# Performance work log

Measured on AMD Instinct MI355X. Metric: run time of the kernel, lower is better.

Reference implementation:

```python
import jax, jax.numpy as jnp
import numpy as np


def setup_inputs() -> dict:
    key = jax.random.key(0)
    B, S, H, O, L, NH = 16, 1024, 1024, 256, 4, 8
    ks = jax.random.split(key, 10)
    s = 0.02
    return {
        "x": jax.random.normal(ks[0], (B, S, H), dtype=jnp.float32),
        "Wf": jax.random.normal(ks[1], (L, H, H), dtype=jnp.float32) * s,
        "bf": jnp.zeros((L, H), dtype=jnp.float32),
        "Wi": jax.random.normal(ks[2], (L, H, H), dtype=jnp.float32) * s,
        "bi": jnp.zeros((L, H), dtype=jnp.float32),
        "Wh": jax.random.normal(ks[3], (L, H, H), dtype=jnp.float32) * s,
        "bh": jnp.zeros((L, H), dtype=jnp.float32),
        "in_proj_w": jax.random.normal(ks[4], (3 * H, H), dtype=jnp.float32) * s,
        "in_proj_b": jnp.zeros((3 * H,), dtype=jnp.float32),
        "out_w": jax.random.normal(ks[5], (H, H), dtype=jnp.float32) * s,
        "out_b": jnp.zeros((H,), dtype=jnp.float32),
        "fc_w": jax.random.normal(ks[6], (O, H), dtype=jnp.float32) * s,
        "fc_b": jnp.zeros((O,), dtype=jnp.float32),
    }


def _min_lstm_layer(x, Wf, bf, Wi, bi, Wh, bh):
    # x: [B, S, D] -> [B, S, H]. minLSTM: h_t = f'_t * h_{t-1} + i'_t * h~_t
    f = jax.nn.sigmoid(jnp.einsum("bsd,hd->bsh", x, Wf) + bf)
    i = jax.nn.sigmoid(jnp.einsum("bsd,hd->bsh", x, Wi) + bi)
    h_tilde = jnp.einsum("bsd,hd->bsh", x, Wh) + bh
    denom = f + i
    fp = f / denom                      # decay coefficient per step
    add = (i / denom) * h_tilde         # input contribution per step
    # sequential scan over time (linear gated recurrence)
    def step(h, inp):
        fp_t, add_t = inp               # each [B, H]
        h = fp_t * h + add_t
        return h, h
    B, S, H = fp.shape
    h0 = jnp.zeros((B, H), dtype=x.dtype)
    _, hs = jax.lax.scan(step, h0, (fp.transpose(1, 0, 2), add.transpose(1, 0, 2)))
    return hs.transpose(1, 0, 2)        # [B, S, H]


def _mhsa(x, in_proj_w, in_proj_b, out_w, out_b, num_heads=8):
    B, S, H = x.shape
    dh = H // num_heads
    qkv = jnp.einsum("bsh,oh->bso", x, in_proj_w) + in_proj_b  # [B,S,3H]
    q, k, v = jnp.split(qkv, 3, axis=-1)
    def heads(t):
        return t.reshape(B, S, num_heads, dh).transpose(0, 2, 1, 3)  # [B,nh,S,dh]
    q, k, v = heads(q), heads(k), heads(v)
    scores = jnp.einsum("bnqd,bnkd->bnqk", q, k) / jnp.sqrt(jnp.float32(dh)).astype(x.dtype)
    attn = jax.nn.softmax(scores, axis=-1)
    o = jnp.einsum("bnqk,bnkd->bnqd", attn, v)
    o = o.transpose(0, 2, 1, 3).reshape(B, S, H)
    return jnp.einsum("bsh,oh->bso", o, out_w) + out_b


def reference(x, Wf, bf, Wi, bi, Wh, bh, in_proj_w, in_proj_b, out_w, out_b, fc_w, fc_b):
    out = x
    L = Wf.shape[0]
    for l in range(L):
        out = _min_lstm_layer(out, Wf[l], bf[l], Wi[l], bi[l], Wh[l], bh[l])
    attn_out = _mhsa(out, in_proj_w, in_proj_b, out_w, out_b, num_heads=8)
    out = attn_out + out                 # dropout is identity at eval
    last = out[:, -1, :]                 # [B, H]
    return jnp.einsum("bh,oh->bo", last, fc_w) + fc_b
```

## Files before the change

### kernel.cpp

```cpp
#include <hip/hip_runtime.h>
#include <hip/hip_bf16.h>
#include <math.h>

#define Bq   16
#define Sq   1024
#define Hq   1024
#define Oq   256
#define Lq   4
#define NHq  8
#define DHq  128
#define Mq   (Bq*Sq)
#define HHq  (Hq*Hq)
#define NCc  32
#define CTc  32

typedef __bf16 bf16x8 __attribute__((ext_vector_type(8)));
typedef float  f32x4  __attribute__((ext_vector_type(4)));

__device__ __forceinline__ float bf2f(unsigned int u) {
    union { unsigned int i; float f; } x; x.i = u << 16; return x.f;
}
__device__ __forceinline__ unsigned short f2bf(float f) {
    union { float f; unsigned int i; } x; x.f = f;
    unsigned int r = x.i + 0x7fffu + ((x.i >> 16) & 1u);
    return (unsigned short)(r >> 16);
}
__device__ __forceinline__ float sigm(float x) { return 1.f / (1.f + __expf(-x)); }

__device__ __forceinline__ void gl2lds16(const unsigned short* g, unsigned short* l) {
    __builtin_amdgcn_global_load_lds((const __attribute__((address_space(1))) void*)g,
                                     (__attribute__((address_space(3))) void*)l, 16, 0, 0);
}

__global__ void cvt_kernel(const float* __restrict__ src, unsigned short* __restrict__ dst, int n) {
    int i = blockIdx.x * 256 + threadIdx.x;
    if (i < n) dst[i] = f2bf(src[i]);
}

__global__ void cvtW_kernel(const float* __restrict__ Wf, const float* __restrict__ Wi,
                            const float* __restrict__ Wh, unsigned short* __restrict__ Wcat) {
    int i = blockIdx.x * 256 + threadIdx.x;
    int l = (i >> 20) / 3;
    int r = i - l * 3 * HHq;
    int g = r >> 20; int j = r & (HHq - 1);
    const float* s = (g == 0) ? Wf : (g == 1) ? Wi : Wh;
    Wcat[i] = f2bf(s[(size_t)l * HHq + j]);
}

__global__ void bias3_kernel(const float* __restrict__ bf_, const float* __restrict__ bi_,
                             const float* __restrict__ bh_, float* __restrict__ out) {
    int i = blockIdx.x * 256 + threadIdx.x;
    int l = i / (3*Hq); int r = i % (3*Hq); int g = r >> 10; int j = r & (Hq-1);
    const float* s = (g == 0) ? bf_ : (g == 1) ? bi_ : bh_;
    out[i] = s[l*Hq + j];
}

__global__ __launch_bounds__(512, 1)
void gemm_gate_kernel(const unsigned short* __restrict__ A, const unsigned short* __restrict__ Wl,
                      const float* __restrict__ bias3, unsigned short* __restrict__ FPo,
                      unsigned short* __restrict__ ADDo)
{
    const int K = Hq;
    __shared__ unsigned short lds[4 * 20480];
    const int tid  = threadIdx.x;

    const int lid = blockIdx.x;
    const int xcd = lid & 7;
    const int s   = lid >> 3;
    const int bm  = xcd * 8 + (s >> 3);
    const int cb  = s & 7;

    const int wid  = tid >> 6, lane = tid & 63;
    const int wm   = (wid >> 2) * 128;
    const int wn   = (wid & 3) * 32;
    const int l15  = lane & 15, quad = lane >> 4;

    const unsigned short* Ag = A + (size_t)(bm*256) * K;

    const int lr   = lane >> 2;
    const int gc   = (lane & 3) ^ ((lane >> 3) & 3);
    int offA[2], ldsA[2];
    #pragma unroll
    for (int q = 0; q < 2; ++q) {
        int ra = wid*32 + q*16 + lr;
        offA[q] = ra * K + gc*8;
        ldsA[q] = (wid*32 + q*16) * 32;
    }
    int offW[3], ldsW[3];
    #pragma unroll
    for (int q = 0; q < 3; ++q) {
        int rw = wid*48 + q*16 + lr;
        int g  = rw >> 7;
        int nr = rw & 127;
        offW[q] = g * HHq + (cb*128 + nr) * K + gc*8;
        ldsW[q] = 8192 + (wid*48 + q*16) * 32;
    }

    const int crd = quad ^ ((l15 >> 1) & 3);

    f32x4 acc[3][8][2] = {};

    auto STAGE = [&](int kt, int slot) {
        const int kof = kt << 5;
        unsigned short* Sb = &lds[slot * 20480];
        #pragma unroll
        for (int q = 0; q < 2; ++q) gl2lds16(Ag + offA[q] + kof, Sb + ldsA[q]);
        #pragma unroll
        for (int q = 0; q < 3; ++q) gl2lds16(Wl + offW[q] + kof, Sb + ldsW[q]);
    };

    auto COMPUTE = [&](int slot) {
        const unsigned short* Sa = &lds[slot * 20480];
        const unsigned short* Sw = Sa + 8192;
        bf16x8 af[8];
        #pragma unroll
        for (int t = 0; t < 8; ++t)
            af[t] = *(const bf16x8*)&Sa[(wm + t*16 + l15)*32 + crd*8];
        __builtin_amdgcn_s_setprio(1);
        #pragma unroll
        for (int g = 0; g < 3; ++g) {
            bf16x8 wf[2];
            #pragma unroll
            for (int t = 0; t < 2; ++t)
                wf[t] = *(const bf16x8*)&Sw[(g*128 + wn + t*16 + l15)*32 + crd*8];
            #pragma unroll
            for (int tm = 0; tm < 8; ++tm)
                #pragma unroll
                for (int tn = 0; tn < 2; ++tn)
                    acc[g][tm][tn] = __builtin_amdgcn_mfma_f32_16x16x32_bf16(af[tm], wf[tn], acc[g][tm][tn], 0, 0, 0);
        }
        __builtin_amdgcn_s_setprio(0);
    };

    const int niter = K >> 5;

    STAGE(0, 0);
    STAGE(1, 1);

    for (int t = 0; t < niter - 2; ++t) {
        STAGE(t + 2, (t + 2) & 3);
        asm volatile("s_waitcnt vmcnt(10) lgkmcnt(0)" ::: "memory");
        __builtin_amdgcn_s_barrier();
        asm volatile("" ::: "memory");
        COMPUTE(t & 3);
    }
    asm volatile("s_waitcnt vmcnt(5) lgkmcnt(0)" ::: "memory");
    __builtin_amdgcn_s_barrier();
    asm volatile("" ::: "memory");
    COMPUTE((niter - 2) & 3);
    asm volatile("s_waitcnt vmcnt(0) lgkmcnt(0)" ::: "memory");
    __builtin_amdgcn_s_barrier();
    asm volatile("" ::: "memory");
    COMPUTE((niter - 1) & 3);

    #pragma unroll
    for (int tm = 0; tm < 8; ++tm) {
        int row0 = bm*256 + wm + tm*16 + quad*4;
        #pragma unroll
        for (int tn = 0; tn < 2; ++tn) {
            int col = cb*128 + wn + tn*16 + l15;
            float bf_ = bias3[col], bi_ = bias3[Hq + col], bh_ = bias3[2*Hq + col];
            #pragma unroll
            for (int r = 0; r < 4; ++r) {
                float f  = sigm(acc[0][tm][tn][r] + bf_);
                float i  = sigm(acc[1][tm][tn][r] + bi_);
                float ht = acc[2][tm][tn][r] + bh_;
                float rd = 1.f / (f + i);
                size_t off = (size_t)(row0 + r) * Hq + col;
                FPo[off]  = f2bf(f * rd);
                ADDo[off] = f2bf(i * rd * ht);
            }
        }
    }
}

__global__ __launch_bounds__(256, 2)
void gemm_bt_kernel(const unsigned short* __restrict__ A, const unsigned short* __restrict__ W,
                    const float* __restrict__ bias, unsigned short* __restrict__ C,
                    int N, int K, int nbn)
{
    __shared__ unsigned short lds[4 * 8192];
    const int tid  = threadIdx.x;

    const int lid = blockIdx.x;
    const int xcd = lid & 7;
    const int s   = lid >> 3;
    const int bm  = xcd * 16 + s / nbn;
    const int bn  = s % nbn;

    const int wid  = tid >> 6, lane = tid & 63;
    const int wm   = (wid >> 1) * 64, wn = (wid & 1) * 64;
    const int l15  = lane & 15, quad = lane >> 4;

    const unsigned short* Ag = A + (size_t)(bm*128) * K;
    const unsigned short* Wg = W + (size_t)(bn*128) * K;

    const int r0   = wid*32 + (lane >> 2);
    const int cst  = (lane & 3) ^ ((r0 >> 1) & 3);
    const int g0   = r0 * K + cst*8;
    const int g1   = (r0 + 16) * K + cst*8;
    const int lofs0 = wid*1024;
    const int lofs1 = wid*1024 + 512;

    const int crd = quad ^ ((l15 >> 1) & 3);

    f32x4 acc[4][4] = {};

    auto STAGE = [&](int kt, int slot) {
        const int kof = kt << 5;
        unsigned short* Sb = &lds[slot * 8192];
        gl2lds16(Ag + g0 + kof, Sb + lofs0);
        gl2lds16(Ag + g1 + kof, Sb + lofs1);
        gl2lds16(Wg + g0 + kof, Sb + 4096 + lofs0);
        gl2lds16(Wg + g1 + kof, Sb + 4096 + lofs1);
    };

    auto COMPUTE = [&](int slot) {
        const unsigned short* Sa = &lds[slot * 8192];
        const unsigned short* Sw = Sa + 4096;
        bf16x8 af[4], wf[4];
        #pragma unroll
        for (int t = 0; t < 4; ++t) {
            af[t] = *(const bf16x8*)&Sa[(wm + t*16 + l15)*32 + crd*8];
            wf[t] = *(const bf16x8*)&Sw[(wn + t*16 + l15)*32 + crd*8];
        }
        __builtin_amdgcn_s_setprio(1);
        #pragma unroll
        for (int tm = 0; tm < 4; ++tm)
            #pragma unroll
            for (int tn = 0; tn < 4; ++tn)
                acc[tm][tn] = __builtin_amdgcn_mfma_f32_16x16x32_bf16(af[tm], wf[tn], acc[tm][tn], 0, 0, 0);
        __builtin_amdgcn_s_setprio(0);
    };

    const int niter = K >> 5;

    STAGE(0, 0);
    STAGE(1, 1);

    for (int it = 0; it < niter - 2; ++it) {
        STAGE(it + 2, (it + 2) & 3);
        asm volatile("s_waitcnt vmcnt(8) lgkmcnt(0)" ::: "memory");
        __builtin_amdgcn_s_barrier();
        asm volatile("" ::: "memory");
        COMPUTE(it & 3);
    }
    asm volatile("s_waitcnt vmcnt(4) lgkmcnt(0)" ::: "memory");
    __builtin_amdgcn_s_barrier();
    asm volatile("" ::: "memory");
    COMPUTE((niter - 2) & 3);
    asm volatile("s_waitcnt vmcnt(0) lgkmcnt(0)" ::: "memory");
    __builtin_amdgcn_s_barrier();
    asm volatile("" ::: "memory");
    COMPUTE((niter - 1) & 3);

    #pragma unroll
    for (int tm = 0; tm < 4; ++tm) {
        int row0 = bm*128 + wm + tm*16 + quad*4;
        #pragma unroll
        for (int tn = 0; tn < 4; ++tn) {
            int col = bn*128 + wn + tn*16 + l15;
            float bv = bias[col];
            #pragma unroll
            for (int r = 0; r < 4; ++r)
                C[(size_t)(row0 + r) * N + col] = f2bf(acc[tm][tn][r] + bv);
        }
    }
}

__global__ __launch_bounds__(256)
void scan_sum_kernel(const unsigned short* __restrict__ FP, const unsigned short* __restrict__ AD,
                     float* __restrict__ Ps, float* __restrict__ Asum) {
    int bid = blockIdx.x;
    int tid = threadIdx.x;
    int b = bid >> 6; int r = bid & 63; int chunk = r >> 1; int jb = r & 1;
    int j = jb*512 + tid*2;
    size_t base = ((size_t)(b*Sq + chunk*CTc)) * Hq + j;
    float P0 = 1.f, P1 = 1.f, A0 = 0.f, A1 = 0.f;
    for (int s = 0; s < CTc; ++s) {
        size_t ro = base + (size_t)s * Hq;
        unsigned int uf = *(const unsigned int*)(FP + ro);
        unsigned int ua = *(const unsigned int*)(AD + ro);
        float fp0 = bf2f(uf & 0xffffu), fp1 = bf2f(uf >> 16);
        float ad0 = bf2f(ua & 0xffffu), ad1 = bf2f(ua >> 16);
        P0 *= fp0; A0 = fp0 * A0 + ad0;
        P1 *= fp1; A1 = fp1 * A1 + ad1;
    }
    int oi = (b*NCc + chunk)*Hq + j;
    Ps[oi] = P0; Ps[oi+1] = P1;
    Asum[oi] = A0; Asum[oi+1] = A1;
}

__global__ void scan_base_kernel(const float* __restrict__ Ps, const float* __restrict__ Asum,
                                 float* __restrict__ Hb) {
    int t = blockIdx.x * 256 + threadIdx.x;
    int b = t >> 10, j = t & 1023;
    float h = 0.f;
    for (int c = 0; c < NCc; ++c) {
        int idx = (b*NCc + c)*Hq + j;
        Hb[idx] = h;
        h = Ps[idx] * h + Asum[idx];
    }
}

__global__ __launch_bounds__(256)
void scan_out_kernel(const unsigned short* __restrict__ FP, const unsigned short* __restrict__ AD,
                     const float* __restrict__ Hb, unsigned short* __restrict__ Ho) {
    int bid = blockIdx.x;
    int tid = threadIdx.x;
    int b = bid >> 6; int r = bid & 63; int chunk = r >> 1; int jb = r & 1;
    int j = jb*512 + tid*2;
    size_t base = ((size_t)(b*Sq + chunk*CTc)) * Hq + j;
    int oi = (b*NCc + chunk)*Hq + j;
    float h0 = Hb[oi], h1 = Hb[oi+1];
    for (int s = 0; s < CTc; ++s) {
        size_t ro = base + (size_t)s * Hq;
        unsigned int uf = *(const unsigned int*)(FP + ro);
        unsigned int ua = *(const unsigned int*)(AD + ro);
        h0 = bf2f(uf & 0xffffu) * h0 + bf2f(ua & 0xffffu);
        h1 = bf2f(uf >> 16)     * h1 + bf2f(ua >> 16);
        unsigned int packed = (unsigned int)f2bf(h0) | ((unsigned int)f2bf(h1) << 16);
        *(unsigned int*)(Ho + ro) = packed;
    }
}

__global__ void xlast_kernel(const unsigned short* __restrict__ act, float* __restrict__ xl) {
    int i = blockIdx.x * 256 + threadIdx.x;
    int b = i >> 10, j = i & 1023;
    xl[i] = bf2f((unsigned int)act[((size_t)(b*Sq + Sq-1)) * Hq + j]);
}

__global__ __launch_bounds__(256)
void gemv_kernel(const float* __restrict__ W, const float* __restrict__ xv,
                 const float* __restrict__ bias, const float* __restrict__ resid,
                 float* __restrict__ out, int N) {
    int b = blockIdx.x;
    int w = threadIdx.x >> 6, lane = threadIdx.x & 63;
    int n = blockIdx.y*4 + w;
    __shared__ float xs[Hq];
    *(float4*)&xs[threadIdx.x*4] = *(const float4*)&xv[(size_t)b*Hq + threadIdx.x*4];
    __syncthreads();
    const float4* wr = (const float4*)(W + (size_t)n * Hq);
    float a = 0.f;
    #pragma unroll
    for (int c = 0; c < 4; ++c) {
        float4 wv = wr[c*64 + lane];
        float4 x4 = *(const float4*)&xs[c*256 + lane*4];
        a += wv.x*x4.x + wv.y*x4.y + wv.z*x4.z + wv.w*x4.w;
    }
    #pragma unroll
    for (int st = 32; st > 0; st >>= 1) a += __shfl_xor(a, st, 64);
    if (lane == 0) out[(size_t)b*N + n] = a + bias[n] + (resid ? resid[(size_t)b*Hq + n] : 0.f);
}

__global__ __launch_bounds__(1024)
void attn_kernel(const unsigned short* __restrict__ KV,
                 const float* __restrict__ q, float* __restrict__ o) {
    int b = blockIdx.x >> 3, nh = blockIdx.x & 7;
    int tid = threadIdx.x;
    __shared__ float qs[DHq];
    __shared__ float p[Sq];
    __shared__ float redw[16];
    __shared__ float red2[16*DHq];
    if (tid < DHq) qs[tid] = q[b*Hq + nh*DHq + tid] * 0.08838834764831845f;
    __syncthreads();

    const int g = tid >> 4, l = tid & 15;
    const unsigned short* Kb = KV + (size_t)b*Sq*2048 + nh*DHq;
    float lmax = -1e30f;
    #pragma unroll 4
    for (int it = 0; it < 16; ++it) {
        int s = it*64 + g;
        union { uint4 v; unsigned short u[8]; } kk;
        kk.v = *(const uint4*)(Kb + (size_t)s*2048 + l*8);
        float a = 0.f;
        #pragma unroll
        for (int j = 0; j < 8; ++j) a += bf2f((unsigned int)kk.u[j]) * qs[l*8 + j];
        a += __shfl_xor(a, 1, 16);
        a += __shfl_xor(a, 2, 16);
        a += __shfl_xor(a, 4, 16);
        a += __shfl_xor(a, 8, 16);
        if (l == 0) p[s] = a;
        lmax = fmaxf(lmax, a);
    }
    #pragma unroll
    for (int st = 32; st > 0; st >>= 1) lmax = fmaxf(lmax, __shfl_xor(lmax, st, 64));
    if ((tid & 63) == 0) redw[tid >> 6] = lmax;
    __syncthreads();
    float mx = redw[0];
    #pragma unroll
    for (int i = 1; i < 16; ++i) mx = fmaxf(mx, redw[i]);

    float e = __expf(p[tid] - mx);
    float ls = e;
    #pragma unroll
    for (int st = 32; st > 0; st >>= 1) ls += __shfl_xor(ls, st, 64);
    __syncthreads();
    p[tid] = e;
    if ((tid & 63) == 0) redw[tid >> 6] = ls;
    __syncthreads();
    float ssum = 0.f;
    #pragma unroll
    for (int i = 0; i < 16; ++i) ssum += redw[i];
    float inv = 1.f / ssum;

    int d2 = (tid & 63) * 2, sb = tid >> 6;
    const unsigned short* Vb = KV + (size_t)b*Sq*2048 + 1024 + nh*DHq + d2;
    float a0 = 0.f, a1 = 0.f;
    for (int s = sb*64; s < sb*64 + 64; ++s) {
        unsigned int vv = *(const unsigned int*)(Vb + (size_t)s*2048);
        float pw = p[s];
        a0 += pw * bf2f(vv & 0xffffu);
        a1 += pw * bf2f(vv >> 16);
    }
    red2[sb*DHq + d2] = a0;
    red2[sb*DHq + d2 + 1] = a1;
    __syncthreads();
    if (tid < DHq) {
        float a = 0.f;
        #pragma unroll
        for (int i = 0; i < 16; ++i) a += red2[i*DHq + tid];
        o[b*Hq + nh*DHq + tid] = a * inv;
    }
}

extern "C" void kernel_launch(void* const* d_in, const int* in_sizes, int n_in,
                              void* d_out, int out_size, void* d_ws, size_t ws_size,
                              hipStream_t stream) {
    const float* x        = (const float*)d_in[0];
    const float* Wf       = (const float*)d_in[1];
    const float* bfv      = (const float*)d_in[2];
    const float* Wi       = (const float*)d_in[3];
    const float* biv      = (const float*)d_in[4];
    const float* Wh       = (const float*)d_in[5];
    const float* bhv      = (const float*)d_in[6];
    const float* in_proj_w= (const float*)d_in[7];
    const float* in_proj_b= (const float*)d_in[8];
    const float* out_w    = (const float*)d_in[9];
    const float* out_b    = (const float*)d_in[10];
    const float* fc_w     = (const float*)d_in[11];
    const float* fc_b     = (const float*)d_in[12];
    float* outp = (float*)d_out;

    char* p = (char*)d_ws;
    auto alloc = [&](size_t bytes) -> void* {
        void* r = (void*)p; p += (bytes + 255) & ~(size_t)255; return r;
    };
    unsigned short* Wcat = (unsigned short*)alloc((size_t)Lq*3*HHq*2);
    unsigned short* Wkv  = (unsigned short*)alloc((size_t)2048*Hq*2);
    float*          Bias3= (float*)alloc((size_t)Lq*3*Hq*4);
    unsigned short* actA = (unsigned short*)alloc((size_t)Mq*Hq*2);
    unsigned short* actB = (unsigned short*)alloc((size_t)Mq*Hq*2);
    unsigned short* FPg  = (unsigned short*)alloc((size_t)Mq*Hq*2);
    unsigned short* ADDg = (unsigned short*)alloc((size_t)Mq*Hq*2);
    float* Ps   = (float*)alloc((size_t)Bq*NCc*Hq*4);
    float* Asum = (float*)alloc((size_t)Bq*NCc*Hq*4);
    float* Hb   = (float*)alloc((size_t)Bq*NCc*Hq*4);
    unsigned short* KV = FPg;
    float* xl   = (float*)alloc((size_t)Bq*Hq*4);
    float* qbuf = (float*)alloc((size_t)Bq*Hq*4);
    float* obuf = (float*)alloc((size_t)Bq*Hq*4);
    float* rbuf = (float*)alloc((size_t)Bq*Hq*4);

    cvt_kernel<<<Mq*Hq/256, 256, 0, stream>>>(x, actA, Mq*Hq);
    cvtW_kernel<<<Lq*3*HHq/256, 256, 0, stream>>>(Wf, Wi, Wh, Wcat);
    cvt_kernel<<<2048*Hq/256, 256, 0, stream>>>(in_proj_w + (size_t)Hq*Hq, Wkv, 2048*Hq);
    bias3_kernel<<<(Lq*3*Hq)/256, 256, 0, stream>>>(bfv, biv, bhv, Bias3);

    unsigned short* cur = actA;
    unsigned short* nxt = actB;
    for (int l = 0; l < Lq; ++l) {
        gemm_gate_kernel<<<(Mq/256)*(Hq/128), 512, 0, stream>>>(
            cur, Wcat + (size_t)l*3*HHq, Bias3 + l*3*Hq, FPg, ADDg);
        scan_sum_kernel<<<Bq*NCc*2, 256, 0, stream>>>(FPg, ADDg, Ps, Asum);
        scan_base_kernel<<<Bq*Hq/256, 256, 0, stream>>>(Ps, Asum, Hb);
        scan_out_kernel<<<Bq*NCc*2, 256, 0, stream>>>(FPg, ADDg, Hb, nxt);
        unsigned short* t = cur; cur = nxt; nxt = t;
    }

    gemm_bt_kernel<<<(Mq/128)*(2048/128), 256, 0, stream>>>(
        cur, Wkv, in_proj_b + Hq, KV, 2048, Hq, 2048/128);
    xlast_kernel<<<Bq*Hq/256, 256, 0, stream>>>(cur, xl);
    gemv_kernel<<<dim3(Bq, Hq/4), 256, 0, stream>>>(in_proj_w, xl, in_proj_b, nullptr, qbuf, Hq);
    attn_kernel<<<Bq*NHq, 1024, 0, stream>>>(KV, qbuf, obuf);
    gemv_kernel<<<dim3(Bq, Hq/4), 256, 0, stream>>>(out_w, obuf, out_b, xl, rbuf, Hq);
    gemv_kernel<<<dim3(Bq, Oq/4), 256, 0, stream>>>(fc_w, rbuf, fc_b, nullptr, outp, Oq);
}
```

Baseline: 842.1 us.

## Fuse chunk scan reduction into gate GEMM epilogue and interleave FP/ADD storage

The gate GEMM epilogue now computes per-32-row chunk products and accumulated sums using in-register accumulation and wave shuffles. It writes Ps/Asum directly, which removes the separate scan_sum kernel and its full re-read of the FP and ADD tensors. FP and ADD are stored interleaved as one 32-bit word, so scan_out reads both with a single vector load. The cost is more epilogue work and register pressure in the GEMM, plus strided 4-byte stores.

```diff
diff --git a/kernel.cpp b/kernel.cpp
--- a/kernel.cpp
+++ b/kernel.cpp
@@ -57,8 +57,8 @@
 
 __global__ __launch_bounds__(512, 1)
 void gemm_gate_kernel(const unsigned short* __restrict__ A, const unsigned short* __restrict__ Wl,
-                      const float* __restrict__ bias3, unsigned short* __restrict__ FPo,
-                      unsigned short* __restrict__ ADDo)
+                      const float* __restrict__ bias3, unsigned int* __restrict__ FA,
+                      float* __restrict__ Ps, float* __restrict__ Asum)
 {
     const int K = Hq;
     __shared__ unsigned short lds[4 * 20480];
@@ -153,22 +153,67 @@
     asm volatile("" ::: "memory");
     COMPUTE((niter - 1) & 3);
 
-    #pragma unroll
-    for (int tm = 0; tm < 8; ++tm) {
-        int row0 = bm*256 + wm + tm*16 + quad*4;
-        #pragma unroll
-        for (int tn = 0; tn < 2; ++tn) {
-            int col = cb*128 + wn + tn*16 + l15;
-            float bf_ = bias3[col], bi_ = bias3[Hq + col], bh_ = bias3[2*Hq + col];
+    const int colc0 = cb*128 + wn + l15;
+    const int colc1 = colc0 + 16;
+    float bf0 = bias3[colc0],      bf1 = bias3[colc1];
+    float bi0 = bias3[Hq+colc0],   bi1 = bias3[Hq+colc1];
+    float bh0 = bias3[2*Hq+colc0], bh1 = bias3[2*Hq+colc1];
+
+    const int b_ = bm >> 2;
+    const int chunkBase = (bm & 3) * 8 + (wm >> 5);
+
+    #pragma unroll
+    for (int cc = 0; cc < 4; ++cc) {
+        float sP[2][2] = {{1.f,1.f},{1.f,1.f}};
+        float sA[2][2] = {{0.f,0.f},{0.f,0.f}};
+        #pragma unroll
+        for (int sg = 0; sg < 2; ++sg) {
+            int tm   = cc*2 + sg;
+            int row0 = bm*256 + wm + tm*16 + quad*4;
             #pragma unroll
             for (int r = 0; r < 4; ++r) {
-                float f  = sigm(acc[0][tm][tn][r] + bf_);
-                float i  = sigm(acc[1][tm][tn][r] + bi_);
-                float ht = acc[2][tm][tn][r] + bh_;
-                float rd = 1.f / (f + i);
-                size_t off = (size_t)(row0 + r) * Hq + col;
-                FPo[off]  = f2bf(f * rd);
-                ADDo[off] = f2bf(i * rd * ht);
+                #pragma unroll
+                for (int tn = 0; tn < 2; ++tn) {
+                    float bfv_ = tn ? bf1 : bf0;
+                    float biv_ = tn ? bi1 : bi0;
+                    float bhv_ = tn ? bh1 : bh0;
+                    int   col  = tn ? colc1 : colc0;
+                    float f  = sigm(acc[0][tm][tn][r] + bfv_);
+                    float i  = sigm(acc[1][tm][tn][r] + biv_);
+                    float ht = acc[2][tm][tn][r] + bhv_;
+                    float rd = 1.f / (f + i);
+                    unsigned short ufp = f2bf(f * rd);
+                    unsigned short uad = f2bf(i * rd * ht);
+                    FA[(size_t)(row0 + r) * Hq + col] =
+                        (unsigned int)ufp | ((unsigned int)uad << 16);
+                    float fpq = bf2f((unsigned int)ufp);
+                    float adq = bf2f((unsigned int)uad);
+                    sA[tn][sg] = fpq * sA[tn][sg] + adq;
+                    sP[tn][sg] *= fpq;
+                }
+            }
+        }
+        int chunk  = chunkBase + cc;
+        int oibase = (b_*NCc + chunk) * Hq;
+        #pragma unroll
+        for (int tn = 0; tn < 2; ++tn) {
+            float P0 = sP[tn][0], A0 = sA[tn][0];
+            float P1 = sP[tn][1], A1 = sA[tn][1];
+            float pp, aa;
+            pp = __shfl_up(P0, 16); aa = __shfl_up(A0, 16);
+            if (quad >= 1) { A0 = P0*aa + A0; P0 = P0*pp; }
+            pp = __shfl_up(P0, 32); aa = __shfl_up(A0, 32);
+            if (quad >= 2) { A0 = P0*aa + A0; P0 = P0*pp; }
+            pp = __shfl_up(P1, 16); aa = __shfl_up(A1, 16);
+            if (quad >= 1) { A1 = P1*aa + A1; P1 = P1*pp; }
+            pp = __shfl_up(P1, 32); aa = __shfl_up(A1, 32);
+            if (quad >= 2) { A1 = P1*aa + A1; P1 = P1*pp; }
+            float P0t = __shfl(P0, 48 + l15); float A0t = __shfl(A0, 48 + l15);
+            float P1t = __shfl(P1, 48 + l15); float A1t = __shfl(A1, 48 + l15);
+            if (quad == 0) {
+                int col = tn ? colc1 : colc0;
+                Ps[oibase + col]   = P1t * P0t;
+                Asum[oibase + col] = P1t * A0t + A1t;
             }
         }
     }
@@ -266,29 +311,6 @@
                 C[(size_t)(row0 + r) * N + col] = f2bf(acc[tm][tn][r] + bv);
         }
     }
-}
-
-__global__ __launch_bounds__(256)
-void scan_sum_kernel(const unsigned short* __restrict__ FP, const unsigned short* __restrict__ AD,
-                     float* __restrict__ Ps, float* __restrict__ Asum) {
-    int bid = blockIdx.x;
-    int tid = threadIdx.x;
-    int b = bid >> 6; int r = bid & 63; int chunk = r >> 1; int jb = r & 1;
-    int j = jb*512 + tid*2;
-    size_t base = ((size_t)(b*Sq + chunk*CTc)) * Hq + j;
-    float P0 = 1.f, P1 = 1.f, A0 = 0.f, A1 = 0.f;
-    for (int s = 0; s < CTc; ++s) {
-        size_t ro = base + (size_t)s * Hq;
-        unsigned int uf = *(const unsigned int*)(FP + ro);
-        unsigned int ua = *(const unsigned int*)(AD + ro);
-        float fp0 = bf2f(uf & 0xffffu), fp1 = bf2f(uf >> 16);
-        float ad0 = bf2f(ua & 0xffffu), ad1 = bf2f(ua >> 16);
-        P0 *= fp0; A0 = fp0 * A0 + ad0;
-        P1 *= fp1; A1 = fp1 * A1 + ad1;
-    }
-    int oi = (b*NCc + chunk)*Hq + j;
-    Ps[oi] = P0; Ps[oi+1] = P1;
-    Asum[oi] = A0; Asum[oi+1] = A1;
 }
 
 __global__ void scan_base_kernel(const float* __restrict__ Ps, const float* __restrict__ Asum,
@@ -304,7 +326,7 @@
 }
 
 __global__ __launch_bounds__(256)
-void scan_out_kernel(const unsigned short* __restrict__ FP, const unsigned short* __restrict__ AD,
+void scan_out_kernel(const unsigned int* __restrict__ FA,
                      const float* __restrict__ Hb, unsigned short* __restrict__ Ho) {
     int bid = blockIdx.x;
     int tid = threadIdx.x;
@@ -315,10 +337,9 @@
     float h0 = Hb[oi], h1 = Hb[oi+1];
     for (int s = 0; s < CTc; ++s) {
         size_t ro = base + (size_t)s * Hq;
-        unsigned int uf = *(const unsigned int*)(FP + ro);
-        unsigned int ua = *(const unsigned int*)(AD + ro);
-        h0 = bf2f(uf & 0xffffu) * h0 + bf2f(ua & 0xffffu);
-        h1 = bf2f(uf >> 16)     * h1 + bf2f(ua >> 16);
+        uint2 v = *(const uint2*)(FA + ro);
+        h0 = bf2f(v.x & 0xffffu) * h0 + bf2f(v.x >> 16);
+        h1 = bf2f(v.y & 0xffffu) * h1 + bf2f(v.y >> 16);
         unsigned int packed = (unsigned int)f2bf(h0) | ((unsigned int)f2bf(h1) << 16);
         *(unsigned int*)(Ho + ro) = packed;
     }
@@ -451,12 +472,11 @@
     float*          Bias3= (float*)alloc((size_t)Lq*3*Hq*4);
     unsigned short* actA = (unsigned short*)alloc((size_t)Mq*Hq*2);
     unsigned short* actB = (unsigned short*)alloc((size_t)Mq*Hq*2);
-    unsigned short* FPg  = (unsigned short*)alloc((size_t)Mq*Hq*2);
-    unsigned short* ADDg = (unsigned short*)alloc((size_t)Mq*Hq*2);
+    unsigned int*   FAg  = (unsigned int*)alloc((size_t)Mq*Hq*4);
     float* Ps   = (float*)alloc((size_t)Bq*NCc*Hq*4);
     float* Asum = (float*)alloc((size_t)Bq*NCc*Hq*4);
     float* Hb   = (float*)alloc((size_t)Bq*NCc*Hq*4);
-    unsigned short* KV = FPg;
+    unsigned short* KV = (unsigned short*)FAg;
     float* xl   = (float*)alloc((size_t)Bq*Hq*4);
     float* qbuf = (float*)alloc((size_t)Bq*Hq*4);
     float* obuf = (float*)alloc((size_t)Bq*Hq*4);
@@ -471,10 +491,9 @@
     unsigned short* nxt = actB;
     for (int l = 0; l < Lq; ++l) {
         gemm_gate_kernel<<<(Mq/256)*(Hq/128), 512, 0, stream>>>(
-            cur, Wcat + (size_t)l*3*HHq, Bias3 + l*3*Hq, FPg, ADDg);
-        scan_sum_kernel<<<Bq*NCc*2, 256, 0, stream>>>(FPg, ADDg, Ps, Asum);
+            cur, Wcat + (size_t)l*3*HHq, Bias3 + l*3*Hq, FAg, Ps, Asum);
         scan_base_kernel<<<Bq*Hq/256, 256, 0, stream>>>(Ps, Asum, Hb);
-        scan_out_kernel<<<Bq*NCc*2, 256, 0, stream>>>(FPg, ADDg, Hb, nxt);
+        scan_out_kernel<<<Bq*NCc*2, 256, 0, stream>>>(FAg, Hb, nxt);
         unsigned short* t = cur; cur = nxt; nxt = t;
     }
 
```

Result: faster. 815.4 us (-3.2%).
